# Performance work log

Hardware: AMD Instinct MI355X
Metric: run time of the kernel (lower is better)

Reference implementation:

```python
import jax, jax.numpy as jnp
import numpy as np

D = 1024      # input_dim == attention_dim == num_heads*head_dim
H = 16        # num_heads
HD = 64       # head_dim
FF = 4096     # ff_dim
EPS = 1e-5


def _layernorm(x, gamma, beta):
    mu = jnp.mean(x, axis=-1, keepdims=True)
    var = jnp.var(x, axis=-1, keepdims=True)
    return (x - mu) * jax.lax.rsqrt(var + EPS) * gamma + beta


def setup_inputs() -> dict:
    key = jax.random.key(0)
    ks = jax.random.split(key, 11)
    s_in = 1.0 / np.sqrt(D)
    s_ff = 1.0 / np.sqrt(FF)
    return {
        "x": jax.random.normal(ks[0], (2, 2048, D), dtype=jnp.float32),
        "w_qkv": jax.random.uniform(ks[1], (D, 3 * D), jnp.float32, -s_in, s_in),
        "b_qkv": jax.random.uniform(ks[2], (3 * D,), jnp.float32, -s_in, s_in),
        "w_o": jax.random.uniform(ks[3], (D, D), jnp.float32, -s_in, s_in),
        "b_o": jax.random.uniform(ks[4], (D,), jnp.float32, -s_in, s_in),
        "g1": jnp.ones((D,), jnp.float32),
        "be1": jnp.zeros((D,), jnp.float32),
        "w1": jax.random.uniform(ks[5], (D, FF), jnp.float32, -s_in, s_in),
        "b1": jax.random.uniform(ks[6], (FF,), jnp.float32, -s_in, s_in),
        "w2": jax.random.uniform(ks[7], (FF, D), jnp.float32, -s_ff, s_ff),
        "b2": jax.random.uniform(ks[8], (D,), jnp.float32, -s_ff, s_ff),
        "g2": jnp.ones((D,), jnp.float32),
        "be2": jnp.zeros((D,), jnp.float32),
    }


def reference(x, w_qkv, b_qkv, w_o, b_o, g1, be1, w1, b1, w2, b2, g2, be2):
    N, L, _ = x.shape
    qkv = x @ w_qkv + b_qkv                       # [N, L, 3D]
    q = qkv[..., :D].reshape(N, L, H, HD)
    k = qkv[..., D:2 * D].reshape(N, L, H, HD)
    v = qkv[..., 2 * D:].reshape(N, L, H, HD)
    scores = jnp.einsum('nqhd,nkhd->nhqk', q, k) / np.sqrt(HD)
    attn = jax.nn.softmax(scores, axis=-1)        # [N, H, L, L]
    out = jnp.einsum('nhql,nlhd->nqhd', attn, v).reshape(N, L, D)
    attn_out = out @ w_o + b_o
    # dropout is identity in eval mode
    h = _layernorm(attn_out + x, g1, be1)
    ff = jax.nn.relu(h @ w1 + b1) @ w2 + b2
    return _layernorm(h + ff, g2, be2)
```

## Files before the change

kernel.cpp:

```cpp
#include <hip/hip_runtime.h>
#include <cstddef>
#include <cstdint>

static constexpr int Dm   = 1024;
static constexpr int Hh   = 16;
static constexpr int HDd  = 64;
static constexpr int FFd  = 4096;
static constexpr int Ls   = 2048;
static constexpr int Nb   = 2;
static constexpr int Mrows = Nb * Ls;

typedef short bf16x8 __attribute__((ext_vector_type(8)));
typedef float f32x4  __attribute__((ext_vector_type(4)));

#if __has_builtin(__builtin_amdgcn_exp2f)
#define EXP2(x) __builtin_amdgcn_exp2f(x)
#else
#define EXP2(x) exp2f(x)
#endif

__device__ __forceinline__ ushort f2b(float f) {
    uint32_t u = __builtin_bit_cast(uint32_t, f);
    u = (u + 0x7FFFu + ((u >> 16) & 1u)) >> 16;
    return (ushort)u;
}
__device__ __forceinline__ ushort f2bf(float f) {
    return (ushort)((__builtin_bit_cast(uint32_t, f) + 0x8000u) >> 16);
}
__device__ __forceinline__ float b2f(ushort b) {
    return __builtin_bit_cast(float, (uint32_t)b << 16);
}

__device__ __forceinline__ void gl2lds16(const ushort* g, ushort* l) {
    __builtin_amdgcn_global_load_lds(
        (const __attribute__((address_space(1))) void*)g,
        (__attribute__((address_space(3))) void*)l, 16, 0, 0);
}

template <int RELU>
__device__ __forceinline__ void pack_store_pair(
    ushort* __restrict__ C, int N, int m0, int n, int lane,
    const f32x4 a, float bv)
{
    float v0 = a[0] + bv, v1 = a[1] + bv, v2 = a[2] + bv, v3 = a[3] + bv;
    if (RELU) {
        v0 = fmaxf(v0, 0.f); v1 = fmaxf(v1, 0.f);
        v2 = fmaxf(v2, 0.f); v3 = fmaxf(v3, 0.f);
    }
    uint32_t a01 = (uint32_t)f2bf(v0) | ((uint32_t)f2bf(v1) << 16);
    uint32_t a23 = (uint32_t)f2bf(v2) | ((uint32_t)f2bf(v3) << 16);
    uint32_t x01 = (uint32_t)__shfl_xor((int)a01, 1);
    uint32_t x23 = (uint32_t)__shfl_xor((int)a23, 1);
    const bool ev = (lane & 1) == 0;
    const uint32_t low  = ev ? a01 : x23;
    const uint32_t high = ev ? x01 : a23;
    const uint32_t dA = (low & 0xFFFFu) | (high << 16);
    const uint32_t dB = (low >> 16) | (high & 0xFFFF0000u);
    const int rb = ev ? 0 : 2;
    const int nc = n - (lane & 1);
    *(uint32_t*)(C + (size_t)(m0 + rb) * N + nc)     = dA;
    *(uint32_t*)(C + (size_t)(m0 + rb + 1) * N + nc) = dB;
}

__global__ __launch_bounds__(256) void prep(
    const float* __restrict__ x, ushort* __restrict__ xb,
    const float* __restrict__ w_qkv, ushort* __restrict__ wqkvT,
    const float* __restrict__ w_o, ushort* __restrict__ woT,
    const float* __restrict__ w1, ushort* __restrict__ w1T,
    const float* __restrict__ w2, ushort* __restrict__ w2T)
{
    __shared__ float t[32][33];
    const int bid = blockIdx.x;
    const int tidx = threadIdx.x;
    if (bid < 4096) {
        const int i = bid * 1024 + tidx * 4;
        float4 v = *(const float4*)(x + i);
        uint2 o;
        o.x = (uint32_t)f2b(v.x) | ((uint32_t)f2b(v.y) << 16);
        o.y = (uint32_t)f2b(v.z) | ((uint32_t)f2b(v.w) << 16);
        *(uint2*)(xb + i) = o;
        return;
    }
    const float* src; ushort* dst; int K, N, r;
    if (bid < 7168)       { r = bid - 4096;  src = w_qkv; dst = wqkvT; K = Dm;  N = 3 * Dm; }
    else if (bid < 8192)  { r = bid - 7168;  src = w_o;   dst = woT;   K = Dm;  N = Dm;  }
    else if (bid < 12288) { r = bid - 8192;  src = w1;    dst = w1T;   K = Dm;  N = FFd; }
    else                  { r = bid - 12288; src = w2;    dst = w2T;   K = FFd; N = Dm;  }
    const int gx = N / 32;
    const int bx = r % gx, by = r / gx;
    const int k0 = by * 32, n0 = bx * 32;
    const int tx = tidx & 31, ty = tidx >> 5;
    #pragma unroll
    for (int i = 0; i < 4; ++i)
        t[ty + i * 8][tx] = src[(size_t)(k0 + ty + i * 8) * N + n0 + tx];
    __syncthreads();
    #pragma unroll
    for (int i = 0; i < 4; ++i)
        dst[(size_t)(n0 + ty + i * 8) * K + k0 + tx] = f2b(t[tx][ty + i * 8]);
}

template <int TN, int RELU, int VOUT, int SPLITK>
__global__ __launch_bounds__(256) void gemm_mfma(
    const ushort* __restrict__ A, const ushort* __restrict__ Bt,
    const float* __restrict__ bias,
    ushort* __restrict__ Cb, ushort* __restrict__ vT, int M, int N, int K)
{
    constexpr int NT  = TN / 32;
    constexpr int BSZ = TN * 32;
    __shared__ __align__(16) ushort As[2 * 128 * 32];
    __shared__ __align__(16) ushort Bs[2 * BSZ];

    const int tid  = threadIdx.x;
    int bx, by;
    {
        const int gx = gridDim.x;
        const int nwg = gx * gridDim.y;
        const int lin = blockIdx.y * gx + blockIdx.x;
        const int swz = (lin & 7) * (nwg >> 3) + (lin >> 3);
        by = swz / gx; bx = swz - by * gx;
    }
    const int bm   = by * 128, bn = bx * TN;
    const int wave = tid >> 6, lane = tid & 63;
    const int wm = (wave & 1) * 64;
    const int wn = (wave >> 1) * (TN / 2);
    const int lr = lane & 15, lq = lane >> 4;

    const int KS   = K / SPLITK;
    const int Koff = (SPLITK > 1) ? blockIdx.z * KS : 0;

    const int rr = wave * 16 + (lane >> 2);
    const int sg = lane & 3;
    const ushort* Ag = A  + (size_t)(bm + rr) * K + Koff + sg * 8;
    const ushort* Bg = Bt + (size_t)(bn + rr) * K + Koff + sg * 8;

    f32x4 acc[4][NT];
    #pragma unroll
    for (int i = 0; i < 4; ++i)
        #pragma unroll
        for (int j = 0; j < NT; ++j)
            acc[i][j] = (f32x4){0.f, 0.f, 0.f, 0.f};

    gl2lds16(Ag,                  As + wave * 512);
    gl2lds16(Ag + (size_t)64 * K, As + 2048 + wave * 512);
    gl2lds16(Bg,                  Bs + wave * 512);
    if (TN == 128)
        gl2lds16(Bg + (size_t)64 * K, Bs + 2048 + wave * 512);
    if (TN == 96) {
        if (wave < 2)
            gl2lds16(Bg + (size_t)64 * K, Bs + 2048 + wave * 512);
    }

    int ib = 0;
    for (int k0 = 0; k0 < KS; k0 += 32, ib ^= 1) {
        __syncthreads();
        if (k0 + 32 < KS) {
            const int nb = ib ^ 1;
            gl2lds16(Ag + k0 + 32,                  As + nb * 4096 + wave * 512);
            gl2lds16(Ag + k0 + 32 + (size_t)64 * K, As + nb * 4096 + 2048 + wave * 512);
            gl2lds16(Bg + k0 + 32,                  Bs + nb * BSZ + wave * 512);
            if (TN == 128)
                gl2lds16(Bg + k0 + 32 + (size_t)64 * K, Bs + nb * BSZ + 2048 + wave * 512);
            if (TN == 96) {
                if (wave < 2)
                    gl2lds16(Bg + k0 + 32 + (size_t)64 * K, Bs + nb * BSZ + 2048 + wave * 512);
            }
        }

        const ushort* Ar = As + ib * 4096;
        const ushort* Br = Bs + ib * BSZ;
        bf16x8 af[4], bf[NT];
        #pragma unroll
        for (int mt = 0; mt < 4; ++mt)
            af[mt] = *(const bf16x8*)(Ar + (wm + mt * 16 + lr) * 32 + lq * 8);
        #pragma unroll
        for (int nt = 0; nt < NT; ++nt)
            bf[nt] = *(const bf16x8*)(Br + (wn + nt * 16 + lr) * 32 + lq * 8);

        #pragma unroll
        for (int mt = 0; mt < 4; ++mt)
            #pragma unroll
            for (int nt = 0; nt < NT; ++nt)
                acc[mt][nt] = __builtin_amdgcn_mfma_f32_16x16x32_bf16(
                    af[mt], bf[nt], acc[mt][nt], 0, 0, 0);
    }

    if (SPLITK > 1) {
        ushort* Cp = Cb + (size_t)blockIdx.z * M * N;
        #pragma unroll
        for (int nt = 0; nt < NT; ++nt) {
            const int n = bn + wn + nt * 16 + lr;
            #pragma unroll
            for (int mt = 0; mt < 4; ++mt)
                pack_store_pair<0>(Cp, N, bm + wm + mt * 16 + lq * 4, n, lane,
                                   acc[mt][nt], 0.0f);
        }
        return;
    }
    if (VOUT) {
        const int batch = bm >> 11;
        #pragma unroll
        for (int nt = 0; nt < NT; ++nt) {
            const int n = bn + wn + nt * 16 + lr;
            const float bv = bias[n];
            if (bn + wn + nt * 16 >= 2 * Dm) {
                const int col = n - 2 * Dm;
                const int h = col >> 6, d = col & 63;
                uint2 p4[4];
                #pragma unroll
                for (int mt = 0; mt < 4; ++mt) {
                    p4[mt].x = (uint32_t)f2bf(acc[mt][nt][0] + bv) |
                               ((uint32_t)f2bf(acc[mt][nt][1] + bv) << 16);
                    p4[mt].y = (uint32_t)f2bf(acc[mt][nt][2] + bv) |
                               ((uint32_t)f2bf(acc[mt][nt][3] + bv) << 16);
                }
                uint2 q4[4];
                #pragma unroll
                for (int mt = 0; mt < 4; ++mt) {
                    q4[mt].x = (uint32_t)__shfl_xor((int)p4[mt].x, 16);
                    q4[mt].y = (uint32_t)__shfl_xor((int)p4[mt].y, 16);
                }
                ushort* drow = vT + (((size_t)(batch * Hh + h)) * HDd + d) * Ls;
                const bool evq = (lq & 1) == 0;
                #pragma unroll
                for (int t = 0; t < 2; ++t) {
                    const int mt = (evq ? 0 : 2) + t;
                    const int key = (bm + wm + mt * 16 + (lq & ~1) * 4) & (Ls - 1);
                    uint4 w;
                    if (evq) w = (uint4){p4[mt].x, p4[mt].y, q4[mt].x, q4[mt].y};
                    else     w = (uint4){q4[mt].x, q4[mt].y, p4[mt].x, p4[mt].y};
                    *(uint4*)(drow + key) = w;
                }
            } else {
                #pragma unroll
                for (int mt = 0; mt < 4; ++mt)
                    pack_store_pair<0>(Cb, N, bm + wm + mt * 16 + lq * 4, n, lane,
                                       acc[mt][nt], bv);
            }
        }
        return;
    }
    #pragma unroll
    for (int nt = 0; nt < NT; ++nt) {
        const int n = bn + wn + nt * 16 + lr;
        const float bv = bias[n];
        #pragma unroll
        for (int mt = 0; mt < 4; ++mt)
            pack_store_pair<RELU>(Cb, N, bm + wm + mt * 16 + lq * 4, n, lane,
                                  acc[mt][nt], bv);
    }
}

__global__ __launch_bounds__(512) void attn_mfma(
    const ushort* __restrict__ qkv, const ushort* __restrict__ vT,
    ushort* __restrict__ out)
{
    const int tid = threadIdx.x, wave = tid >> 6, lane = tid & 63;
    const int g = wave >> 2, wv = wave & 3;
    const int lr = lane & 15, lq = lane >> 4;
    int bx, h, n;
    {
        const int lin = (blockIdx.z * 16 + blockIdx.y) * 16 + blockIdx.x;
        const int swz = (lin & 7) * 64 + (lin >> 3);
        bx = swz & 15; h = (swz >> 4) & 15; n = swz >> 8;
    }
    const int q0 = bx * 128 + wv * 32;
    const int kt0 = g * (Ls / 2);
    const size_t RS = 3 * Dm;
    const ushort* base  = qkv + (size_t)n * Ls * RS;
    const ushort* vbase = vT + (size_t)(n * Hh + h) * HDd * Ls;

    __shared__ __align__(16) ushort KV[4][64 * 72];
    __shared__ __align__(16) float cmb[34][256];
    ushort* Kb = KV[2 * g];
    ushort* Vt = KV[2 * g + 1];

    bf16x8 qf[2][2];
    {
        const float c = 0.18033688011112042f;
        #pragma unroll
        for (int qh = 0; qh < 2; ++qh) {
            const ushort* qg = base + (size_t)(q0 + qh * 16 + lr) * RS + h * HDd + lq * 8;
            bf16x8 t0 = *(const bf16x8*)(qg);
            bf16x8 t1 = *(const bf16x8*)(qg + 32);
            #pragma unroll
            for (int j = 0; j < 8; ++j) {
                qf[0][qh][j] = (short)f2b(b2f((ushort)t0[j]) * c);
                qf[1][qh][j] = (short)f2b(b2f((ushort)t1[j]) * c);
            }
        }
    }

    bf16x8 onesf;
    #pragma unroll
    for (int j = 0; j < 8; ++j) onesf[j] = (short)0x3F80;
    const f32x4 z4 = (f32x4){0.f, 0.f, 0.f, 0.f};

    f32x4 o[4][2];
    #pragma unroll
    for (int dt = 0; dt < 4; ++dt)
        #pragma unroll
        for (int qh = 0; qh < 2; ++qh)
            o[dt][qh] = (f32x4){0.f, 0.f, 0.f, 0.f};
    f32x4 dacc[2];
    dacc[0] = (f32x4){0.f, 0.f, 0.f, 0.f};
    dacc[1] = (f32x4){0.f, 0.f, 0.f, 0.f};

    const int lt = tid & 255;
    const int srow = lt >> 2, ssg = lt & 3;
    const ushort* kg = base + (size_t)srow * RS + Dm + h * HDd;
    const ushort* vg = vbase + (size_t)srow * Ls;

    const int sA = (((2 * ssg) & 3) * 8) + (((ssg >> 1) & 1) * 4);
    const int sB = (((2 * ssg + 1) & 3) * 8) + (((ssg >> 1) & 1) * 4);

    int4 ka = *(const int4*)(kg + (size_t)kt0 * RS + ssg * 8);
    int4 kb = *(const int4*)(kg + (size_t)kt0 * RS + (ssg + 4) * 8);
    int4 va = *(const int4*)(vg + kt0 + ssg * 8);
    int4 vb = *(const int4*)(vg + kt0 + (ssg + 4) * 8);

    for (int kt = kt0; kt < kt0 + Ls / 2; kt += 64) {
        __syncthreads();
        *(int4*)(Kb + srow * 72 + ssg * 8)       = ka;
        *(int4*)(Kb + srow * 72 + (ssg + 4) * 8) = kb;
        {
            ushort* vrow = Vt + srow * 72;
            *(uint2*)(vrow + sA)      = (uint2){(uint32_t)va.x, (uint32_t)va.y};
            *(uint2*)(vrow + sB)      = (uint2){(uint32_t)va.z, (uint32_t)va.w};
            *(uint2*)(vrow + 32 + sA) = (uint2){(uint32_t)vb.x, (uint32_t)vb.y};
            *(uint2*)(vrow + 32 + sB) = (uint2){(uint32_t)vb.z, (uint32_t)vb.w};
        }
        __syncthreads();

        if (kt + 64 < kt0 + Ls / 2) {
            const ushort* kp = kg + (size_t)(kt + 64) * RS;
            const ushort* vp = vg + (kt + 64);
            ka = *(const int4*)(kp + ssg * 8);
            kb = *(const int4*)(kp + (ssg + 4) * 8);
            va = *(const int4*)(vp + ssg * 8);
            vb = *(const int4*)(vp + (ssg + 4) * 8);
        }

        f32x4 s[4][2];
        #pragma unroll
        for (int ks = 0; ks < 2; ++ks)
            #pragma unroll
            for (int mt = 0; mt < 4; ++mt) {
                bf16x8 kf = *(const bf16x8*)(Kb + (mt * 16 + lr) * 72 + ks * 32 + lq * 8);
                #pragma unroll
                for (int qh = 0; qh < 2; ++qh)
                    s[mt][qh] = __builtin_amdgcn_mfma_f32_16x16x32_bf16(
                        kf, qf[ks][qh], ks == 0 ? z4 : s[mt][qh], 0, 0, 0);
            }

        uint2 pb[4][2];
        #pragma unroll
        for (int mt = 0; mt < 4; ++mt)
            #pragma unroll
            for (int qh = 0; qh < 2; ++qh) {
                float p0 = EXP2(s[mt][qh][0]);
                float p1 = EXP2(s[mt][qh][1]);
                float p2 = EXP2(s[mt][qh][2]);
                float p3 = EXP2(s[mt][qh][3]);
                uint32_t w0, w1;
                asm("v_cvt_pk_bf16_f32 %0, %1, %2" : "=v"(w0) : "v"(p0), "v"(p1));
                asm("v_cvt_pk_bf16_f32 %0, %1, %2" : "=v"(w1) : "v"(p2), "v"(p3));
                pb[mt][qh].x = w0;
                pb[mt][qh].y = w1;
            }

        #pragma unroll
        for (int ks = 0; ks < 2; ++ks) {
            bf16x8 pf[2];
            #pragma unroll
            for (int qh = 0; qh < 2; ++qh) {
                uint4 u = (uint4){pb[2 * ks][qh].x, pb[2 * ks][qh].y,
                                  pb[2 * ks + 1][qh].x, pb[2 * ks + 1][qh].y};
                pf[qh] = __builtin_bit_cast(bf16x8, u);
            }
            #pragma unroll
            for (int dt = 0; dt < 4; ++dt) {
                bf16x8 vf = *(const bf16x8*)(Vt + (dt * 16 + lr) * 72 + ks * 32 + lq * 8);
                #pragma unroll
                for (int qh = 0; qh < 2; ++qh)
                    o[dt][qh] = __builtin_amdgcn_mfma_f32_16x16x32_bf16(
                        vf, pf[qh], o[dt][qh], 0, 0, 0);
            }
            #pragma unroll
            for (int qh = 0; qh < 2; ++qh)
                dacc[qh] = __builtin_amdgcn_mfma_f32_16x16x32_bf16(
                    onesf, pf[qh], dacc[qh], 0, 0, 0);
        }
    }

    const int c = wv * 64 + lane;
    __syncthreads();
    if (g == 1) {
        #pragma unroll
        for (int dt = 0; dt < 4; ++dt)
            #pragma unroll
            for (int qh = 0; qh < 2; ++qh)
                #pragma unroll
                for (int r = 0; r < 4; ++r)
                    cmb[dt * 8 + qh * 4 + r][c] = o[dt][qh][r];
        cmb[32][c] = dacc[0][0];
        cmb[33][c] = dacc[1][0];
    }
    __syncthreads();
    if (g == 0) {
        #pragma unroll
        for (int dt = 0; dt < 4; ++dt)
            #pragma unroll
            for (int qh = 0; qh < 2; ++qh)
                #pragma unroll
                for (int r = 0; r < 4; ++r)
                    o[dt][qh][r] += cmb[dt * 8 + qh * 4 + r][c];
        const float d0 = dacc[0][0] + cmb[32][c];
        const float d1 = dacc[1][0] + cmb[33][c];
        #pragma unroll
        for (int qh = 0; qh < 2; ++qh) {
            const float inv = 1.0f / (qh == 0 ? d0 : d1);
            ushort* orow = out + (size_t)(n * Ls + q0 + qh * 16 + lr) * Dm + h * HDd;
            #pragma unroll
            for (int dt = 0; dt < 4; ++dt) {
                ushort4 ob;
                ushort* op = (ushort*)&ob;
                #pragma unroll
                for (int r = 0; r < 4; ++r) op[r] = f2bf(o[dt][qh][r] * inv);
                *(ushort4*)(orow + dt * 16 + lq * 4) = ob;
            }
        }
    }
}

template <int NP, int OTHER_BF16, int OUT_F32>
__global__ __launch_bounds__(256) void addn_ln(
    const ushort* __restrict__ part, const void* __restrict__ other,
    const float* __restrict__ bias,
    const float* __restrict__ gamma, const float* __restrict__ beta,
    float* __restrict__ outf, ushort* __restrict__ outb)
{
    const int row = blockIdx.x;
    const int tid = threadIdx.x;

    float4 bv = ((const float4*)bias)[tid];
    float v[4];
    if (OTHER_BF16) {
        ushort4 u = ((const ushort4*)((const ushort*)other + (size_t)row * Dm))[tid];
        v[0] = b2f(u.x) + bv.x; v[1] = b2f(u.y) + bv.y;
        v[2] = b2f(u.z) + bv.z; v[3] = b2f(u.w) + bv.w;
    } else {
        float4 f = ((const float4*)((const float*)other + (size_t)row * Dm))[tid];
        v[0] = f.x + bv.x; v[1] = f.y + bv.y; v[2] = f.z + bv.z; v[3] = f.w + bv.w;
    }
    #pragma unroll
    for (int pp = 0; pp < NP; ++pp) {
        ushort4 u = ((const ushort4*)(part + (size_t)pp * Mrows * Dm
                                           + (size_t)row * Dm))[tid];
        v[0] += b2f(u.x); v[1] += b2f(u.y); v[2] += b2f(u.z); v[3] += b2f(u.w);
    }

    float s  = v[0] + v[1] + v[2] + v[3];
    float sq = v[0]*v[0] + v[1]*v[1] + v[2]*v[2] + v[3]*v[3];

    __shared__ float red[8];
    #pragma unroll
    for (int off = 32; off > 0; off >>= 1) {
        s  += __shfl_down(s, off);
        sq += __shfl_down(sq, off);
    }
    const int wv = tid >> 6;
    if ((tid & 63) == 0) { red[wv] = s; red[4 + wv] = sq; }
    __syncthreads();
    s  = red[0] + red[1] + red[2] + red[3];
    sq = red[4] + red[5] + red[6] + red[7];

    const float mu  = s * (1.0f / Dm);
    const float var = sq * (1.0f / Dm) - mu * mu;
    const float inv = rsqrtf(var + 1e-5f);

    const float4 g  = ((const float4*)gamma)[tid];
    const float4 be = ((const float4*)beta)[tid];
    float ov[4];
    ov[0] = (v[0] - mu) * inv * g.x + be.x;
    ov[1] = (v[1] - mu) * inv * g.y + be.y;
    ov[2] = (v[2] - mu) * inv * g.z + be.z;
    ov[3] = (v[3] - mu) * inv * g.w + be.w;
    if (OUT_F32) {
        float4 o4 = {ov[0], ov[1], ov[2], ov[3]};
        ((float4*)(outf + (size_t)row * Dm))[tid] = o4;
    } else {
        uint2 ob;
        ob.x = (uint32_t)f2bf(ov[0]) | ((uint32_t)f2bf(ov[1]) << 16);
        ob.y = (uint32_t)f2bf(ov[2]) | ((uint32_t)f2bf(ov[3]) << 16);
        *(uint2*)(outb + (size_t)row * Dm + tid * 4) = ob;
    }
}

extern "C" void kernel_launch(void* const* d_in, const int* in_sizes, int n_in,
                              void* d_out, int out_size, void* d_ws, size_t ws_size,
                              hipStream_t stream)
{
    const float* x     = (const float*)d_in[0];
    const float* w_qkv = (const float*)d_in[1];
    const float* b_qkv = (const float*)d_in[2];
    const float* w_o   = (const float*)d_in[3];
    const float* b_o   = (const float*)d_in[4];
    const float* g1    = (const float*)d_in[5];
    const float* be1   = (const float*)d_in[6];
    const float* w1    = (const float*)d_in[7];
    const float* b1    = (const float*)d_in[8];
    const float* w2    = (const float*)d_in[9];
    const float* b2    = (const float*)d_in[10];
    const float* g2    = (const float*)d_in[11];
    const float* be2   = (const float*)d_in[12];
    float* out = (float*)d_out;

    char* p = (char*)d_ws;
    ushort* part4 = (ushort*)p;  p += (size_t)4 * Mrows * Dm * 2;
    ushort* qkvb  = (ushort*)p;  p += (size_t)Mrows * 3 * Dm * 2;
    ushort* hb    = (ushort*)p;  p += (size_t)Mrows * Dm * 2;
    ushort* ffb   = (ushort*)p;  p += (size_t)Mrows * FFd * 2;
    ushort* wqkvT = (ushort*)p;  p += (size_t)(3 * Dm) * Dm * 2;
    ushort* woT   = (ushort*)p;  p += (size_t)Dm * Dm * 2;
    ushort* w1T   = (ushort*)p;  p += (size_t)FFd * Dm * 2;
    ushort* w2T   = (ushort*)p;  p += (size_t)Dm * FFd * 2;
    ushort* vTg   = (ushort*)p;  p += (size_t)Mrows * Dm * 2;

    ushort* attnb = part4 + (size_t)2 * Mrows * Dm;
    ushort* xb    = part4 + (size_t)3 * Mrows * Dm;

    prep<<<dim3(16384), dim3(256), 0, stream>>>(
        x, xb, w_qkv, wqkvT, w_o, woT, w1, w1T, w2, w2T);

    gemm_mfma<96, 0, 1, 1><<<dim3(3 * Dm / 96, Mrows / 128), dim3(256), 0, stream>>>(
        xb, wqkvT, b_qkv, qkvb, vTg, Mrows, 3 * Dm, Dm);

    attn_mfma<<<dim3(Ls / 128, Hh, Nb), dim3(512), 0, stream>>>(qkvb, vTg, attnb);

    gemm_mfma<64, 0, 0, 2><<<dim3(Dm / 64, Mrows / 128, 2), dim3(256), 0, stream>>>(
        attnb, woT, nullptr, part4, nullptr, Mrows, Dm, Dm);

    addn_ln<2, 0, 0><<<dim3(Mrows), dim3(256), 0, stream>>>(
        part4, x, b_o, g1, be1, nullptr, hb);

    gemm_mfma<128, 1, 0, 1><<<dim3(FFd / 128, Mrows / 128), dim3(256), 0, stream>>>(
        hb, w1T, b1, ffb, nullptr, Mrows, FFd, Dm);

    gemm_mfma<128, 0, 0, 4><<<dim3(Dm / 128, Mrows / 128, 4), dim3(256), 0, stream>>>(
        ffb, w2T, nullptr, part4, nullptr, Mrows, Dm, FFd);

    addn_ln<4, 1, 1><<<dim3(Mrows), dim3(256), 0, stream>>>(
        part4, hb, b2, g2, be2, out, nullptr);
}
```

Before: 359.5 us.

## Add 256x256-tile triple-buffered MFMA GEMM for both FFN matmuls

Adds a new 512-thread GEMM kernel with 256x256 output tiles and a 32-wide K step. It uses a three-stage LDS ring filled by direct global-to-LDS loads, an XOR-swizzled LDS layout and raised wave priority around the MFMA blocks. The FFN up-projection (with bias and ReLU) and the split-K down-projection now use this kernel instead of the 128-tile GEMM. The aim is more data reuse per byte loaded and fewer blocks. The cost is about 96KB of LDS and heavy register use per block, which limits occupancy to roughly one block per CU and leaves a single wave of 256 blocks, so tail and latency hiding become more sensitive.

```diff
diff --git a/kernel.cpp b/kernel.cpp
--- a/kernel.cpp
+++ b/kernel.cpp
@@ -250,6 +250,126 @@
     }
 }
 
+template <int RELU, int SPLITK>
+__global__ __launch_bounds__(512, 2) void gemm256(
+    const ushort* __restrict__ A, const ushort* __restrict__ Bt,
+    const float* __restrict__ bias, ushort* __restrict__ Cb,
+    int M, int N, int K)
+{
+    __shared__ __align__(16) ushort As3[3][256 * 32];
+    __shared__ __align__(16) ushort Bs3[3][256 * 32];
+
+    const int tid = threadIdx.x, wave = tid >> 6, lane = tid & 63;
+    const int lr = lane & 15, lq = lane >> 4;
+    const int wm2 = wave >> 2, wn2 = wave & 3;
+
+    int bx, by;
+    {
+        const int gx = gridDim.x;
+        const int nwg = gx * gridDim.y;
+        const int lin = blockIdx.y * gx + blockIdx.x;
+        const int swz = (lin & 7) * (nwg >> 3) + (lin >> 3);
+        by = swz / gx; bx = swz - by * gx;
+    }
+    const int bm = by * 256, bn = bx * 256;
+    const int KS = K / SPLITK;
+    const int Koff = (SPLITK > 1) ? blockIdx.z * KS : 0;
+    const int nt = KS / 32;
+
+    int srow[2], scbS[2];
+    #pragma unroll
+    for (int j = 0; j < 2; ++j) {
+        const int c = (wave * 2 + j) * 64 + lane;
+        const int row = c >> 2, cb = c & 3;
+        srow[j] = row;
+        scbS[j] = cb ^ ((row ^ (row >> 2)) & 3);
+    }
+
+    f32x4 acc[8][4];
+    #pragma unroll
+    for (int i = 0; i < 8; ++i)
+        #pragma unroll
+        for (int j = 0; j < 4; ++j)
+            acc[i][j] = (f32x4){0.f, 0.f, 0.f, 0.f};
+
+    #define STAGE(t)                                                          \
+        do {                                                                  \
+            const int b_ = (t) % 3;                                           \
+            _Pragma("unroll")                                                 \
+            for (int j_ = 0; j_ < 2; ++j_) {                                  \
+                gl2lds16(A + (size_t)(bm + srow[j_]) * K + Koff + (t) * 32    \
+                           + scbS[j_] * 8,                                    \
+                         As3[b_] + (wave * 2 + j_) * 512);                    \
+                gl2lds16(Bt + (size_t)(bn + srow[j_]) * K + Koff + (t) * 32   \
+                           + scbS[j_] * 8,                                    \
+                         Bs3[b_] + (wave * 2 + j_) * 512);                    \
+            }                                                                 \
+        } while (0)
+
+    STAGE(0);
+    STAGE(1);
+
+    for (int t = 0; t < nt; ++t) {
+        if (t + 1 < nt) asm volatile("s_waitcnt vmcnt(4)" ::: "memory");
+        else            asm volatile("s_waitcnt vmcnt(0)" ::: "memory");
+        asm volatile("s_barrier" ::: "memory");
+        if (t + 2 < nt) STAGE(t + 2);
+
+        const ushort* Ar = As3[t % 3];
+        const ushort* Br = Bs3[t % 3];
+        #pragma unroll
+        for (int q = 0; q < 4; ++q) {
+            const int qm = q >> 1, qn = q & 1;
+            bf16x8 af[4], bf[2];
+            #pragma unroll
+            for (int i = 0; i < 4; ++i) {
+                const int r = wm2 * 128 + (qm * 4 + i) * 16 + lr;
+                af[i] = *(const bf16x8*)(Ar + r * 32
+                            + (lq ^ ((r ^ (r >> 2)) & 3)) * 8);
+            }
+            #pragma unroll
+            for (int i = 0; i < 2; ++i) {
+                const int r = wn2 * 64 + (qn * 2 + i) * 16 + lr;
+                bf[i] = *(const bf16x8*)(Br + r * 32
+                            + (lq ^ ((r ^ (r >> 2)) & 3)) * 8);
+            }
+            __builtin_amdgcn_s_setprio(1);
+            #pragma unroll
+            for (int i = 0; i < 4; ++i)
+                #pragma unroll
+                for (int k2 = 0; k2 < 2; ++k2)
+                    acc[qm * 4 + i][qn * 2 + k2] =
+                        __builtin_amdgcn_mfma_f32_16x16x32_bf16(
+                            af[i], bf[k2], acc[qm * 4 + i][qn * 2 + k2], 0, 0, 0);
+            __builtin_amdgcn_s_setprio(0);
+        }
+    }
+    #undef STAGE
+
+    if (SPLITK > 1) {
+        ushort* Cp = Cb + (size_t)blockIdx.z * M * N;
+        #pragma unroll
+        for (int mi = 0; mi < 8; ++mi) {
+            const int m0 = bm + wm2 * 128 + mi * 16 + lq * 4;
+            #pragma unroll
+            for (int ni = 0; ni < 4; ++ni) {
+                const int n = bn + wn2 * 64 + ni * 16 + lr;
+                pack_store_pair<0>(Cp, N, m0, n, lane, acc[mi][ni], 0.0f);
+            }
+        }
+        return;
+    }
+    #pragma unroll
+    for (int mi = 0; mi < 8; ++mi) {
+        const int m0 = bm + wm2 * 128 + mi * 16 + lq * 4;
+        #pragma unroll
+        for (int ni = 0; ni < 4; ++ni) {
+            const int n = bn + wn2 * 64 + ni * 16 + lr;
+            pack_store_pair<RELU>(Cb, N, m0, n, lane, acc[mi][ni], bias[n]);
+        }
+    }
+}
+
 __global__ __launch_bounds__(512) void attn_mfma(
     const ushort* __restrict__ qkv, const ushort* __restrict__ vT,
     ushort* __restrict__ out)
@@ -543,11 +663,11 @@
     addn_ln<2, 0, 0><<<dim3(Mrows), dim3(256), 0, stream>>>(
         part4, x, b_o, g1, be1, nullptr, hb);
 
-    gemm_mfma<128, 1, 0, 1><<<dim3(FFd / 128, Mrows / 128), dim3(256), 0, stream>>>(
-        hb, w1T, b1, ffb, nullptr, Mrows, FFd, Dm);
-
-    gemm_mfma<128, 0, 0, 4><<<dim3(Dm / 128, Mrows / 128, 4), dim3(256), 0, stream>>>(
-        ffb, w2T, nullptr, part4, nullptr, Mrows, Dm, FFd);
+    gemm256<1, 1><<<dim3(FFd / 256, Mrows / 256), dim3(512), 0, stream>>>(
+        hb, w1T, b1, ffb, Mrows, FFd, Dm);
+
+    gemm256<0, 4><<<dim3(Dm / 256, Mrows / 256, 4), dim3(512), 0, stream>>>(
+        ffb, w2T, nullptr, part4, Mrows, Dm, FFd);
 
     addn_ln<4, 1, 1><<<dim3(Mrows), dim3(256), 0, stream>>>(
         part4, hb, b2, g2, be2, out, nullptr);
```

New measurement: 355.5 us. Within noise of the previous version (-1.1%).
